# Performance work log

Measured on AMD Instinct MI355X. Metric: run time of the kernel, lower is better.

The kernel has to match this reference:

```python
import jax, jax.numpy as jnp
import numpy as np

B = 1024            # number of graphs
C = (64, 32, 16, 1) # args.channels
K = 25              # args.kernel_size
CUTOFF = 0.5        # args.cutoff
EPS = 1e-15


def gmm_conv(x, pos, n, g, mu, sigma, root, bias, out_ch):
    """GMMConv over a dynamically-built radius graph (dist<CUTOFF, no self loops),
    with mean aggregation, expressed densely per-graph (n in {5,25,75}).
    Equivalent to getA()+PyG GMMConv(aggr='mean') scatter/gather."""
    nb = pos.shape[0] // n
    posb = pos.reshape(nb, n, 2)
    # diff[b, s, t] = pos_t - pos_s  (edge (row=s, col=t): message flows s -> t)
    diff = posb[:, None, :, :] - posb[:, :, None, :]
    dist = jnp.linalg.norm(diff + 1e-12, axis=-1)            # [B,n,n]
    mask = (dist < CUTOFF) & (~jnp.eye(n, dtype=bool))       # [B,n,n]
    pseudo = diff / CUTOFF + 0.5                             # [B,n,n,2] edge_attr
    # Gaussian kernel weights: exp(-0.5 * sum_d (u_d - mu_kd)^2 / sigma_kd^2)
    gauss = jnp.exp(-0.5 * jnp.sum((pseudo[..., None, :] - mu) ** 2
                                   / (sigma ** 2 + EPS), axis=-1))  # [B,n,n,K]
    w = gauss * mask[..., None]
    xm = (x @ g).reshape(nb, n, K, out_ch)                   # source-transformed feats
    agg = jnp.einsum('bstk,bsko->bto', w, xm)                # scatter-sum into targets
    deg = jnp.maximum(jnp.sum(mask, axis=1), 1)              # in-degree per target [B,n]
    out = agg / deg[..., None].astype(x.dtype)               # mean aggregation
    return out.reshape(-1, out_ch) + x @ root + bias


def setup_inputs() -> dict:
    key = jax.random.key(0)
    ks = jax.random.split(key, 40)
    inp = {}
    inp['x'] = jax.random.normal(ks[0], (B * 5, C[0]), jnp.float32)
    inp['pos'] = jax.random.uniform(ks[1], (B * 5, 2), jnp.float32)

    def conv_params(k, fin, fout):
        k1, k2, k3, k4, k5 = jax.random.split(k, 5)
        g = jax.random.normal(k1, (fin, K * fout), jnp.float32) / np.sqrt(fin)
        mu = jax.random.normal(k2, (K, 2), jnp.float32)
        sigma = jax.random.uniform(k3, (K, 2), jnp.float32, minval=0.5, maxval=1.5)
        root = jax.random.normal(k4, (fin, fout), jnp.float32) / np.sqrt(fin)
        bias = jax.random.normal(k5, (fout,), jnp.float32) * 0.01
        return g, mu, sigma, root, bias

    for i, (fin, fout) in enumerate([(C[0], 5 * C[1]), (C[1], 3 * C[2]), (C[2], C[3])], 1):
        g, mu, sigma, root, bias = conv_params(ks[1 + i], fin, fout)
        inp[f'g{i}'], inp[f'mu{i}'], inp[f'sig{i}'] = g, mu, sigma
        inp[f'root{i}'], inp[f'cb{i}'] = root, bias

    def lin(k, fin, fout):
        kw, kb = jax.random.split(k)
        return (jax.random.normal(kw, (fin, fout), jnp.float32) / np.sqrt(fin),
                jax.random.normal(kb, (fout,), jnp.float32) * 0.01)

    for j, (pre, dims) in enumerate([('p1', (2 + C[1], 128, 64, 2)),
                                     ('p2', (2 + C[2], 128, 64, 2))]):
        for li in range(3):
            w, b_ = lin(ks[10 + 3 * j + li], dims[li], dims[li + 1])
            inp[f'{pre}w{li+1}'], inp[f'{pre}b{li+1}'] = w, b_
    return inp


def reference(x, pos, g1, mu1, sig1, root1, cb1, g2, mu2, sig2, root2, cb2,
              g3, mu3, sig3, root3, cb3,
              p1w1, p1b1, p1w2, p1b2, p1w3, p1b3,
              p2w1, p2b1, p2w2, p2b2, p2w3, p2b3):
    elu = jax.nn.elu
    # stage 1: 5 nodes/graph, conv expands node count x5
    x = elu(gmm_conv(x, pos, 5, g1, mu1, sig1, root1, cb1, 5 * C[1])).reshape(-1, C[1])
    p = jnp.concatenate([jnp.repeat(pos, 5, axis=0), x], axis=1)
    p = elu(p @ p1w1 + p1b1)
    p = elu(p @ p1w2 + p1b2)
    pos = elu(p @ p1w3 + p1b3)
    # stage 2: 25 nodes/graph, conv expands node count x3
    x = elu(gmm_conv(x, pos, 25, g2, mu2, sig2, root2, cb2, 3 * C[2])).reshape(-1, C[2])
    p = jnp.concatenate([jnp.repeat(pos, 3, axis=0), x], axis=1)
    p = elu(p @ p2w1 + p2b1)
    p = elu(p @ p2w2 + p2b2)
    pos = elu(p @ p2w3 + p2b3)
    # stage 3: 75 nodes/graph
    x = jnp.tanh(gmm_conv(x, pos, 75, g3, mu3, sig3, root3, cb3, C[3])).reshape(-1, C[3])
    return x, pos
```

## Files before the change

### kernel.cpp

```cpp
#include <hip/hip_runtime.h>
#include <math.h>


__device__ __forceinline__ float eluf(float v) { return v > 0.f ? v : __expf(v) - 1.f; }

#define NLOG2E_HALF (-0.72134752f)

__global__ __launch_bounds__(512) void conv1_kernel(
    const float* __restrict__ x, const float* __restrict__ pos,
    const float* __restrict__ g, const float* __restrict__ mu, const float* __restrict__ sig,
    const float* __restrict__ root, const float* __restrict__ bias,
    float* __restrict__ xout)
{
  const int b = blockIdx.x, tid = threadIdx.x;
  __shared__ __align__(16) float s_xT[64 * 12];
  __shared__ __align__(16) float s_xm[10 * 832];
  __shared__ __align__(16) float s_w[2 * 5 * 5 * 28];
  __shared__ __align__(16) float s_red[2 * 2 * 5 * 160];
  __shared__ float s_pos[20];
  __shared__ float s_msc[25][4];
  __shared__ float s_ideg[10];

  if (tid < 20) s_pos[tid] = pos[b * 20 + tid];
  if (tid < 25) {
    float m0 = mu[2 * tid], m1 = mu[2 * tid + 1];
    float s0 = sig[2 * tid], s1 = sig[2 * tid + 1];
    s_msc[tid][0] = 0.5f - m0;
    s_msc[tid][1] = 0.5f - m1;
    s_msc[tid][2] = NLOG2E_HALF / (s0 * s0 + 1e-15f);
    s_msc[tid][3] = NLOG2E_HALF / (s1 * s1 + 1e-15f);
  }
  for (int e = tid; e < 640; e += 512) { int nd = e >> 6, i = e & 63; s_xT[i * 12 + nd] = x[b * 640 + nd * 64 + i]; }
  for (int e = tid; e < 320; e += 512) { int r = e / 32, c = e % 32; s_xm[r * 832 + 800 + c] = 0.f; }
  __syncthreads();

  if (tid < 10) {
    int gg = tid / 5, t = tid % 5, c = 0;
    for (int s = 0; s < 5; ++s) {
      if (s == t) continue;
      float d0 = s_pos[(gg * 5 + t) * 2]     - s_pos[(gg * 5 + s) * 2]     + 1e-12f;
      float d1 = s_pos[(gg * 5 + t) * 2 + 1] - s_pos[(gg * 5 + s) * 2 + 1] + 1e-12f;
      c += (d0 * d0 + d1 * d1 < 0.25f) ? 1 : 0;
    }
    s_ideg[tid] = 1.f / (float)(c < 1 ? 1 : c);
  }
  for (int e = tid; e < 1400; e += 512) {
    int gg = e / 700, r2 = e % 700, t = r2 / 140, c = r2 % 140;
    int ch = c / 28, skl = c % 28;
    float wv = 0.f;
    if (skl < 25) {
      int kk = skl / 5, s = skl % 5, k = ch * 5 + kk;
      float d0 = s_pos[(gg * 5 + t) * 2]     - s_pos[(gg * 5 + s) * 2];
      float d1 = s_pos[(gg * 5 + t) * 2 + 1] - s_pos[(gg * 5 + s) * 2 + 1];
      float e0 = d0 + 1e-12f, e1 = d1 + 1e-12f;
      bool m = (e0 * e0 + e1 * e1 < 0.25f) && (s != t);
      float q0 = fmaf(2.f, d0, s_msc[k][0]);
      float q1 = fmaf(2.f, d1, s_msc[k][1]);
      float a = q0 * q0 * s_msc[k][2];
      a = fmaf(q1 * q1, s_msc[k][3], a);
// ... 39 lines not shown
    }
    __syncthreads();
    if (tid < 320) {
#define C1_STEP(SK0) { \
      float2 m0 = *(const float2*)&s_xm[(sg * 5 + ((SK0) % 5)) * 832 + ((SK0) / 5) * 160 + so0]; \
      float2 m1 = *(const float2*)&s_xm[(sg * 5 + (((SK0) + 1) % 5)) * 832 + (((SK0) + 1) / 5) * 160 + so0]; \
      float2 m2 = *(const float2*)&s_xm[(sg * 5 + (((SK0) + 2) % 5)) * 832 + (((SK0) + 2) / 5) * 160 + so0]; \
      float2 m3 = *(const float2*)&s_xm[(sg * 5 + (((SK0) + 3) % 5)) * 832 + (((SK0) + 3) / 5) * 160 + so0]; \
      _Pragma("unroll") \
      for (int t = 0; t < 5; ++t) { \
        const float4 wv = *(const float4*)&s_w[((sg * 5 + t) * 5 + ch) * 28 + (SK0)]; \
        sacc[t][0] = fmaf(wv.x, m0.x, sacc[t][0]); sacc[t][1] = fmaf(wv.x, m0.y, sacc[t][1]); \
        sacc[t][0] = fmaf(wv.y, m1.x, sacc[t][0]); sacc[t][1] = fmaf(wv.y, m1.y, sacc[t][1]); \
        sacc[t][0] = fmaf(wv.z, m2.x, sacc[t][0]); sacc[t][1] = fmaf(wv.z, m2.y, sacc[t][1]); \
        sacc[t][0] = fmaf(wv.w, m3.x, sacc[t][0]); sacc[t][1] = fmaf(wv.w, m3.y, sacc[t][1]); \
      } }
      if (sks == 0) { C1_STEP(0) C1_STEP(4) C1_STEP(8) C1_STEP(12) }
      else          { C1_STEP(16) C1_STEP(20) C1_STEP(24) }
#undef C1_STEP
    }
    __syncthreads();
  }

  if (tid < 400) {
    const int rb = tid / 80, cb = tid % 80;
    const int r0 = rb * 2, c0 = cb * 2;
    float a00 = 0.f, a01 = 0.f, a10 = 0.f, a11 = 0.f;
    #pragma unroll 4
    for (int i = 0; i < 64; ++i) {
      float2 rv = *(const float2*)(root + i * 160 + c0);
      float2 xv = *(const float2*)&s_xT[i * 12 + r0];
      a00 = fmaf(xv.x, rv.x, a00); a01 = fmaf(xv.x, rv.y, a01);
      a10 = fmaf(xv.y, rv.x, a10); a11 = fmaf(xv.y, rv.y, a11);
    }
    *(float2*)&s_xm[r0 * 832 + c0]       = make_float2(a00, a01);
    *(float2*)&s_xm[(r0 + 1) * 832 + c0] = make_float2(a10, a11);
  }
  if (tid < 320) {
    #pragma unroll
    for (int t = 0; t < 5; ++t) {
      s_red[((sks * 2 + sg) * 5 + t) * 160 + so0]     = sacc[t][0];
      s_red[((sks * 2 + sg) * 5 + t) * 160 + so0 + 1] = sacc[t][1];
    }
  }
  __syncthreads();
  for (int e = tid; e < 1600; e += 512) {
    int gg = e / 800, r2 = e % 800, t = r2 / 160, o = r2 % 160;
    float v = s_red[(gg * 5 + t) * 160 + o] + s_red[((2 + gg) * 5 + t) * 160 + o];
    v = v * s_ideg[gg * 5 + t] + s_xm[(gg * 5 + t) * 832 + o] + bias[o];
    xout[b * 1600 + e] = eluf(v);
  }
}

__global__ __launch_bounds__(320) void conv2_kernel(
    const float* __restrict__ x, const float* __restrict__ pos,
    const float* __restrict__ g, const float* __restrict__ mu, const float* __restrict__ sig,
    const float* __restrict__ root, const float* __restrict__ bias,
    float* __restrict__ xout)
{
  const int b = blockIdx.x, tid = threadIdx.x;
  __shared__ __align__(16) float s_xT[32 * 28];
  __shared__ __align__(16) float s_xm[125 * 52];
  __shared__ __align__(16) float s_w[25 * 132];
  __shared__ __align__(8)  float2 s_u[25 * 26];
  __shared__ float s_ek[25 * 5];
  __shared__ float s_pos[50];
  __shared__ float s_ideg[25];

  if (tid < 50) s_pos[tid] = pos[b * 50 + tid];
  if (tid < 25) {
    float m0 = mu[2 * tid], m1 = mu[2 * tid + 1];
    float sg0 = sig[2 * tid], sg1 = sig[2 * tid + 1];
    float n0 = NLOG2E_HALF / (sg0 * sg0 + 1e-15f);
    float n1 = NLOG2E_HALF / (sg1 * sg1 + 1e-15f);
    float c0 = 0.5f - m0, c1 = 0.5f - m1;
    s_ek[tid * 5 + 0] = n0;
    s_ek[tid * 5 + 1] = n1;
    s_ek[tid * 5 + 2] = 2.f * n0 * c0;
    s_ek[tid * 5 + 3] = 2.f * n1 * c1;
    s_ek[tid * 5 + 4] = fmaf(n0, c0 * c0, n1 * c1 * c1);
  }
  for (int e = tid; e < 800; e += 320) { int r = e / 32, i = e % 32; s_xT[i * 28 + r] = x[b * 800 + e]; }
  __syncthreads();

  for (int e = tid; e < 625; e += 320) {
    int t = e / 25, s = e % 25;
    float d0 = s_pos[t * 2]     - s_pos[s * 2];
    float d1 = s_pos[t * 2 + 1] - s_pos[s * 2 + 1];
    float e0 = d0 + 1e-12f, e1 = d1 + 1e-12f;
    bool m = (e0 * e0 + e1 * e1 < 0.25f) && (s != t);
    s_u[t * 26 + s] = m ? make_float2(2.f * d0, 2.f * d1) : make_float2(1e18f, 0.f);
  }
  if (tid < 25) {
    int t = tid, c = 0;
    for (int s = 0; s < 25; ++s) {
      if (s == t) continue;
      float d0 = s_pos[t * 2]     - s_pos[s * 2]     + 1e-12f;
      float d1 = s_pos[t * 2 + 1] - s_pos[s * 2 + 1] + 1e-12f;
      c += (d0 * d0 + d1 * d1 < 0.25f) ? 1 : 0;
    }
    s_ideg[t] = 1.f / (float)(c < 1 ? 1 : c);
  }
  __syncthreads();

  const bool act = tid < 300;
  const int grp = tid / 60, rr = tid % 60, tg = rr / 12, og = rr % 12;
  const int o0 = og * 4;
  const int t0 = tg * 5, sk0 = grp * 25, s0 = tg * 5;

  float acc2[5][4];
  #pragma unroll
  for (int tt = 0; tt < 5; ++tt) { acc2[tt][0] = acc2[tt][1] = acc2[tt][2] = acc2[tt][3] = 0.f; }

  for (int ch = 0; ch < 5; ++ch) {
    const int k0 = ch * 5;
    for (int e = tid; e < 3125; e += 320) {
      int t = e / 125, c = e % 125;
      int kk = c / 25, s = c % 25, k = k0 + kk;
      float2 uv = s_u[t * 26 + s];
      const float* ekp = &s_ek[k * 5];
      float ar = fmaf(uv.x * uv.x, ekp[0],
                 fmaf(uv.y * uv.y, ekp[1],
                 fmaf(uv.x, ekp[2],
                 fmaf(uv.y, ekp[3], ekp[4]))));
      s_w[t * 132 + c] = exp2f(ar);
    }
    if (act) {
      const float* gp = g + (k0 + grp) * 48 + o0;
      float a[5][4];
      #pragma unroll
      for (int r = 0; r < 5; ++r) { a[r][0] = a[r][1] = a[r][2] = a[r][3] = 0.f; }
      #pragma unroll 4
      for (int i = 0; i < 32; ++i) {
        float4 gv = *(const float4*)(gp + i * 1200);
        float x0 = s_xT[i * 28 + s0];
        float x1 = s_xT[i * 28 + s0 + 1];
        float x2 = s_xT[i * 28 + s0 + 2];
        float x3 = s_xT[i * 28 + s0 + 3];
        float x4 = s_xT[i * 28 + s0 + 4];
        a[0][0] = fmaf(x0, gv.x, a[0][0]); a[0][1] = fmaf(x0, gv.y, a[0][1]);
        a[0][2] = fmaf(x0, gv.z, a[0][2]); a[0][3] = fmaf(x0, gv.w, a[0][3]);
        a[1][0] = fmaf(x1, gv.x, a[1][0]); a[1][1] = fmaf(x1, gv.y, a[1][1]);
        a[1][2] = fmaf(x1, gv.z, a[1][2]); a[1][3] = fmaf(x1, gv.w, a[1][3]);
        a[2][0] = fmaf(x2, gv.x, a[2][0]); a[2][1] = fmaf(x2, gv.y, a[2][1]);
        a[2][2] = fmaf(x2, gv.z, a[2][2]); a[2][3] = fmaf(x2, gv.w, a[2][3]);
        a[3][0] = fmaf(x3, gv.x, a[3][0]); a[3][1] = fmaf(x3, gv.y, a[3][1]);
        a[3][2] = fmaf(x3, gv.z, a[3][2]); a[3][3] = fmaf(x3, gv.w, a[3][3]);
        a[4][0] = fmaf(x4, gv.x, a[4][0]); a[4][1] = fmaf(x4, gv.y, a[4][1]);
        a[4][2] = fmaf(x4, gv.z, a[4][2]); a[4][3] = fmaf(x4, gv.w, a[4][3]);
      }
      #pragma unroll
      for (int j = 0; j < 5; ++j)
        *(float4*)&s_xm[(grp * 25 + s0 + j) * 52 + o0] = make_float4(a[j][0], a[j][1], a[j][2], a[j][3]);
    }
    __syncthreads();
    if (act) {
      #pragma unroll 5
      for (int q = 0; q < 25; ++q) {
        const int sk = sk0 + q;
        float4 mv = *(const float4*)&s_xm[sk * 52 + o0];
        float w0 = s_w[(t0 + 0) * 132 + sk];
        float w1 = s_w[(t0 + 1) * 132 + sk];
        float w2 = s_w[(t0 + 2) * 132 + sk];
        float w3 = s_w[(t0 + 3) * 132 + sk];
        float w4 = s_w[(t0 + 4) * 132 + sk];
        acc2[0][0] = fmaf(w0, mv.x, acc2[0][0]); acc2[0][1] = fmaf(w0, mv.y, acc2[0][1]);
        acc2[0][2] = fmaf(w0, mv.z, acc2[0][2]); acc2[0][3] = fmaf(w0, mv.w, acc2[0][3]);
        acc2[1][0] = fmaf(w1, mv.x, acc2[1][0]); acc2[1][1] = fmaf(w1, mv.y, acc2[1][1]);
        acc2[1][2] = fmaf(w1, mv.z, acc2[1][2]); acc2[1][3] = fmaf(w1, mv.w, acc2[1][3]);
        acc2[2][0] = fmaf(w2, mv.x, acc2[2][0]); acc2[2][1] = fmaf(w2, mv.y, acc2[2][1]);
        acc2[2][2] = fmaf(w2, mv.z, acc2[2][2]); acc2[2][3] = fmaf(w2, mv.w, acc2[2][3]);
        acc2[3][0] = fmaf(w3, mv.x, acc2[3][0]); acc2[3][1] = fmaf(w3, mv.y, acc2[3][1]);
        acc2[3][2] = fmaf(w3, mv.z, acc2[3][2]); acc2[3][3] = fmaf(w3, mv.w, acc2[3][3]);
        acc2[4][0] = fmaf(w4, mv.x, acc2[4][0]); acc2[4][1] = fmaf(w4, mv.y, acc2[4][1]);
        acc2[4][2] = fmaf(w4, mv.z, acc2[4][2]); acc2[4][3] = fmaf(w4, mv.w, acc2[4][3]);
      }
    }
    __syncthreads();
  }

  if (act) {
    #pragma unroll
    for (int tt = 0; tt < 5; ++tt)
      *(float4*)&s_xm[grp * 1200 + (t0 + tt) * 48 + o0] =
          make_float4(acc2[tt][0], acc2[tt][1], acc2[tt][2], acc2[tt][3]);
  }
  __syncthreads();
  for (int e = tid; e < 1200; e += 320) {
    int t = e / 48, o = e % 48;
    float v = s_xm[e] + s_xm[1200 + e] + s_xm[2400 + e] + s_xm[3600 + e] + s_xm[4800 + e];
    v *= s_ideg[t];
    #pragma unroll 8
    for (int i = 0; i < 32; ++i) v = fmaf(s_xT[i * 28 + t], root[i * 48 + o], v);
    xout[b * 1200 + e] = eluf(v + bias[o]);
  }
}

__global__ __launch_bounds__(384) void conv3_kernel(
    const float* __restrict__ x, const float* __restrict__ pos,
    const float* __restrict__ g, const float* __restrict__ mu, const float* __restrict__ sig,
    const float* __restrict__ root, const float* __restrict__ bias,
    float* __restrict__ xout)
{
  const int b = blockIdx.x, tid = threadIdx.x;
  __shared__ __align__(8) float2 s_u[75 * 75];
  __shared__ float s_xm[75 * 28];
  __shared__ float s_x[75 * 16];
  __shared__ float s_g3[400];
  __shared__ float s_pos[150];
  __shared__ float s_ek[25 * 5];
  __shared__ float s_ideg[75];
  __shared__ float s_out[75];
  __shared__ float s_r3[16];

  if (tid < 150) s_pos[tid] = pos[b * 150 + tid];
  for (int e = tid; e < 1200; e += 384) s_x[e] = x[b * 1200 + e];
  for (int e = tid; e < 400; e += 384) s_g3[e] = g[e];
  if (tid < 25) {
    float m0 = mu[2 * tid], m1 = mu[2 * tid + 1];
    float sg0 = sig[2 * tid], sg1 = sig[2 * tid + 1];
    float n0 = NLOG2E_HALF / (sg0 * sg0 + 1e-15f);
    float n1 = NLOG2E_HALF / (sg1 * sg1 + 1e-15f);
    float c0 = 0.5f - m0, c1 = 0.5f - m1;
    s_ek[tid * 5 + 0] = n0;
    s_ek[tid * 5 + 1] = n1;
    s_ek[tid * 5 + 2] = 2.f * n0 * c0;
    s_ek[tid * 5 + 3] = 2.f * n1 * c1;
    s_ek[tid * 5 + 4] = n0 * c0 * c0 + n1 * c1 * c1;
  }
  if (tid < 16) s_r3[tid] = root[tid];
  if (tid < 75) s_out[tid] = 0.f;
  __syncthreads();

  for (int e = tid; e < 1875; e += 384) {
    int s = e / 25, k = e % 25;
    float a = 0.f;
    #pragma unroll
    for (int i = 0; i < 16; ++i) a = fmaf(s_x[s * 16 + i], s_g3[i * 25 + k], a);
    s_xm[s * 28 + k] = a;
  }
  for (int e = tid; e < 5625; e += 384) {
    int t = e / 75, s = e % 75;
    float d0 = s_pos[t * 2]     - s_pos[s * 2];
    float d1 = s_pos[t * 2 + 1] - s_pos[s * 2 + 1];
    float e0 = d0 + 1e-12f, e1 = d1 + 1e-12f;
    bool m = (e0 * e0 + e1 * e1 < 0.25f) && (s != t);
    s_u[e] = m ? make_float2(2.f * d0, 2.f * d1) : make_float2(1e18f, 0.f);
  }
  if (tid < 75) {
    int t = tid, c = 0;
    for (int s = 0; s < 75; ++s) {
      if (s == t) continue;
      float d0 = s_pos[t * 2]     - s_pos[s * 2]     + 1e-12f;
      float d1 = s_pos[t * 2 + 1] - s_pos[s * 2 + 1] + 1e-12f;
      c += (d0 * d0 + d1 * d1 < 0.25f) ? 1 : 0;
    }
    s_ideg[t] = 1.f / (float)(c < 1 ? 1 : c);
  }
  __syncthreads();

  if (tid < 375) {
    const int t = tid / 5, kg = tid % 5;
    float n0[5], n1[5], e0[5], e1[5], f[5];
    #pragma unroll
    for (int j = 0; j < 5; ++j) {
      int k = kg * 5 + j;
      n0[j] = s_ek[k * 5 + 0]; n1[j] = s_ek[k * 5 + 1];
      e0[j] = s_ek[k * 5 + 2]; e1[j] = s_ek[k * 5 + 3];
      f[j]  = s_ek[k * 5 + 4];
    }
    float acc[5] = {0.f, 0.f, 0.f, 0.f, 0.f};
    for (int s = 0; s < 75; ++s) {
      float2 uv = s_u[t * 75 + s];
      float u00 = uv.x * uv.x, u11 = uv.y * uv.y;
      #pragma unroll
      for (int j = 0; j < 5; ++j) {
        float ar = fmaf(u00, n0[j], fmaf(u11, n1[j], fmaf(uv.x, e0[j], fmaf(uv.y, e1[j], f[j]))));
        acc[j] = fmaf(exp2f(ar), s_xm[s * 28 + kg * 5 + j], acc[j]);
      }
    }
    float sum = acc[0] + acc[1] + acc[2] + acc[3] + acc[4];
    atomicAdd(&s_out[t], sum);
  }
  __syncthreads();

  if (tid < 75) {
    int t = tid;
    float r = 0.f;
    #pragma unroll
    for (int i = 0; i < 16; ++i) r = fmaf(s_x[t * 16 + i], s_r3[i], r);
    xout[b * 75 + t] = tanhf(s_out[t] * s_ideg[t] + r + bias[0]);
  }
}

__global__ __launch_bounds__(256) void mlp_kernel(
    const float* __restrict__ pos_src, const float* __restrict__ feat,
    const float* __restrict__ w1, const float* __restrict__ b1,
    const float* __restrict__ w2, const float* __restrict__ b2,
    const float* __restrict__ w3, const float* __restrict__ b3,
    float* __restrict__ out, int fdim, int rep)
{
  const int tid = threadIdx.x;
  const int row0 = blockIdx.x * 64;
  const int din = fdim + 2;
  __shared__ __align__(16) float s_inT[34][68];
  __shared__ __align__(16) float s_h1T[128][68];
  __shared__ __align__(16) float s_h2T[64][68];

  if (tid < 128) {
    int r = tid >> 1, d = tid & 1;
    s_inT[d][r] = pos_src[((row0 + r) / rep) * 2 + d];
  }
  for (int e = tid; e < 64 * fdim; e += 256) {
    int r = e / fdim, c = e % fdim;
    s_inT[2 + c][r] = feat[(row0 + r) * fdim + c];
  }
  __syncthreads();

  {
    const int rb = tid >> 4, jb = tid & 15;
    const int r0 = rb << 2, j0 = jb << 3;
    float acc[4][8];
    #pragma unroll
    for (int jj = 0; jj < 8; ++jj) {
      float bv = b1[j0 + jj];
      acc[0][jj] = bv; acc[1][jj] = bv; acc[2][jj] = bv; acc[3][jj] = bv;
    }
    for (int i = 0; i < din; ++i) {
      float4 xa = *(const float4*)&s_inT[i][r0];
      float4 wa = *(const float4*)(w1 + i * 128 + j0);
      float4 wb = *(const float4*)(w1 + i * 128 + j0 + 4);
      float wv[8] = {wa.x, wa.y, wa.z, wa.w, wb.x, wb.y, wb.z, wb.w};
      #pragma unroll
      for (int jj = 0; jj < 8; ++jj) {
        acc[0][jj] = fmaf(xa.x, wv[jj], acc[0][jj]);
        acc[1][jj] = fmaf(xa.y, wv[jj], acc[1][jj]);
        acc[2][jj] = fmaf(xa.z, wv[jj], acc[2][jj]);
        acc[3][jj] = fmaf(xa.w, wv[jj], acc[3][jj]);
      }
    }
    #pragma unroll
    for (int jj = 0; jj < 8; ++jj)
      *(float4*)&s_h1T[j0 + jj][r0] =
        make_float4(eluf(acc[0][jj]), eluf(acc[1][jj]), eluf(acc[2][jj]), eluf(acc[3][jj]));
  }
  __syncthreads();

  {
    const int rb = tid >> 4, jb = tid & 15;
    const int r0 = rb << 2, j0 = jb << 2;
    float acc[4][4];
    #pragma unroll
    for (int jj = 0; jj < 4; ++jj) {
      float bv = b2[j0 + jj];
      acc[0][jj] = bv; acc[1][jj] = bv; acc[2][jj] = bv; acc[3][jj] = bv;
    }
    #pragma unroll 4
    for (int i = 0; i < 128; ++i) {
      float4 ha = *(const float4*)&s_h1T[i][r0];
      float4 wa = *(const float4*)(w2 + i * 64 + j0);
      float wv[4] = {wa.x, wa.y, wa.z, wa.w};
      #pragma unroll
      for (int jj = 0; jj < 4; ++jj) {
        acc[0][jj] = fmaf(ha.x, wv[jj], acc[0][jj]);
        acc[1][jj] = fmaf(ha.y, wv[jj], acc[1][jj]);
        acc[2][jj] = fmaf(ha.z, wv[jj], acc[2][jj]);
        acc[3][jj] = fmaf(ha.w, wv[jj], acc[3][jj]);
      }
    }
    #pragma unroll
    for (int jj = 0; jj < 4; ++jj)
      *(float4*)&s_h2T[j0 + jj][r0] =
        make_float4(eluf(acc[0][jj]), eluf(acc[1][jj]), eluf(acc[2][jj]), eluf(acc[3][jj]));
  }
  __syncthreads();

  if (tid < 128) {
    int r = tid >> 1, c = tid & 1;
    float a = b3[c];
    #pragma unroll 8
    for (int j = 0; j < 64; ++j)
      a = fmaf(s_h2T[j][r], w3[j * 2 + c], a);
    out[(row0 + r) * 2 + c] = eluf(a);
  }
}

extern "C" void kernel_launch(void* const* d_in, const int* in_sizes, int n_in,
                              void* d_out, int out_size, void* d_ws, size_t ws_size,
                              hipStream_t stream)
{
  const float* x     = (const float*)d_in[0];
  const float* pos   = (const float*)d_in[1];
  const float* g1    = (const float*)d_in[2];
  const float* mu1   = (const float*)d_in[3];
  const float* sig1  = (const float*)d_in[4];
  const float* root1 = (const float*)d_in[5];
  const float* cb1   = (const float*)d_in[6];
  const float* g2    = (const float*)d_in[7];
  const float* mu2   = (const float*)d_in[8];
  const float* sig2  = (const float*)d_in[9];
  const float* root2 = (const float*)d_in[10];
  const float* cb2   = (const float*)d_in[11];
  const float* g3    = (const float*)d_in[12];
  const float* mu3   = (const float*)d_in[13];
  const float* sig3  = (const float*)d_in[14];
  const float* root3 = (const float*)d_in[15];
  const float* cb3   = (const float*)d_in[16];
  const float* p1w1  = (const float*)d_in[17];
  const float* p1b1  = (const float*)d_in[18];
  const float* p1w2  = (const float*)d_in[19];
  const float* p1b2  = (const float*)d_in[20];
  const float* p1w3  = (const float*)d_in[21];
  const float* p1b3  = (const float*)d_in[22];
  const float* p2w1  = (const float*)d_in[23];
  const float* p2b1  = (const float*)d_in[24];
  const float* p2w2  = (const float*)d_in[25];
  const float* p2b2  = (const float*)d_in[26];
  const float* p2w3  = (const float*)d_in[27];
  const float* p2b3  = (const float*)d_in[28];

  float* out  = (float*)d_out;
  float* ws   = (float*)d_ws;
  float* x1   = ws;
  float* pos1 = ws + 819200;
  float* x2   = ws + 870400;
  float* x3   = out;
  float* pos2 = out + 76800;

  conv1_kernel<<<dim3(512), dim3(512), 0, stream>>>(x, pos, g1, mu1, sig1, root1, cb1, x1);
  mlp_kernel<<<dim3(400), dim3(256), 0, stream>>>(pos, x1, p1w1, p1b1, p1w2, p1b2, p1w3, p1b3,
                                                  pos1, 32, 5);
  conv2_kernel<<<dim3(1024), dim3(320), 0, stream>>>(x1, pos1, g2, mu2, sig2, root2, cb2, x2);
  mlp_kernel<<<dim3(1200), dim3(256), 0, stream>>>(pos1, x2, p2w1, p2b1, p2w2, p2b2, p2w3, p2b3,
                                                  pos2, 16, 3);
  conv3_kernel<<<dim3(1024), dim3(384), 0, stream>>>(x2, pos2, g3, mu3, sig3, root3, cb3, x3);
}
```

Before: 336.6 us.

## Warp-specialize conv2 with double-buffered per-kernel build, shrink MLP tiles, recompute conv3 edges

Conv2 now splits its threads into roles. Threads 128 and up build the Gaussian weights and the transformed features for the next kernel component into a second buffer, while the first 128 threads accumulate the current component. This replaces the old five-chunk loop that carried two barriers per chunk, and it cuts shared memory use. The MLP kernel moves to 32-row tiles so it launches twice as many blocks with a smaller shared footprint. Conv3 drops its precomputed 75x75 edge array and recomputes the pairwise offsets inline to save shared memory. The trade-off is 25 barrier-separated iterations, with only 120 of 256 threads doing the accumulation.

```diff
diff --git a/kernel.cpp b/kernel.cpp
--- a/kernel.cpp
+++ b/kernel.cpp
@@ -5,6 +5,10 @@
 __device__ __forceinline__ float eluf(float v) { return v > 0.f ? v : __expf(v) - 1.f; }
 
 #define NLOG2E_HALF (-0.72134752f)
+
+#define FMA4(A, S, V) \
+  A.x = fmaf(S, V.x, A.x); A.y = fmaf(S, V.y, A.y); \
+  A.z = fmaf(S, V.z, A.z); A.w = fmaf(S, V.w, A.w);
 
 __global__ __launch_bounds__(512) void conv1_kernel(
     const float* __restrict__ x, const float* __restrict__ pos,
@@ -150,22 +154,26 @@
   }
 }
 
-__global__ __launch_bounds__(320) void conv2_kernel(
+__global__ __launch_bounds__(256) void conv2_kernel(
     const float* __restrict__ x, const float* __restrict__ pos,
     const float* __restrict__ g, const float* __restrict__ mu, const float* __restrict__ sig,
     const float* __restrict__ root, const float* __restrict__ bias,
     float* __restrict__ xout)
 {
   const int b = blockIdx.x, tid = threadIdx.x;
-  __shared__ __align__(16) float s_xT[32 * 28];
-  __shared__ __align__(16) float s_xm[125 * 52];
-  __shared__ __align__(16) float s_w[25 * 132];
+  __shared__ __align__(16) float s_x[25 * 36];
+  __shared__ __align__(16) float s_xm[2 * 28 * 52];
+  __shared__ __align__(16) float s_w[2 * 25 * 28];
   __shared__ __align__(8)  float2 s_u[25 * 26];
-  __shared__ float s_ek[25 * 5];
-  __shared__ float s_pos[50];
+  __shared__ float s_ek[125];
   __shared__ float s_ideg[25];
 
-  if (tid < 50) s_pos[tid] = pos[b * 50 + tid];
+  const float* posb = pos + b * 50;
+  for (int e = tid; e < 800; e += 256) s_x[(e >> 5) * 36 + (e & 31)] = x[b * 800 + e];
+  for (int e = tid; e < 312; e += 256) {
+    int q = e / 52, cc = e % 52;
+    s_xm[(q / 3) * 1456 + (25 + q % 3) * 52 + cc] = 0.f;
+  }
   if (tid < 25) {
     float m0 = mu[2 * tid], m1 = mu[2 * tid + 1];
     float sg0 = sig[2 * tid], sg1 = sig[2 * tid + 1];
@@ -178,13 +186,10 @@
     s_ek[tid * 5 + 3] = 2.f * n1 * c1;
     s_ek[tid * 5 + 4] = fmaf(n0, c0 * c0, n1 * c1 * c1);
   }
-  for (int e = tid; e < 800; e += 320) { int r = e / 32, i = e % 32; s_xT[i * 28 + r] = x[b * 800 + e]; }
-  __syncthreads();
-
-  for (int e = tid; e < 625; e += 320) {
+  for (int e = tid; e < 625; e += 256) {
     int t = e / 25, s = e % 25;
-    float d0 = s_pos[t * 2]     - s_pos[s * 2];
-    float d1 = s_pos[t * 2 + 1] - s_pos[s * 2 + 1];
+    float d0 = posb[t * 2]     - posb[s * 2];
+    float d1 = posb[t * 2 + 1] - posb[s * 2 + 1];
     float e0 = d0 + 1e-12f, e1 = d1 + 1e-12f;
     bool m = (e0 * e0 + e1 * e1 < 0.25f) && (s != t);
     s_u[t * 26 + s] = m ? make_float2(2.f * d0, 2.f * d1) : make_float2(1e18f, 0.f);
@@ -193,104 +198,102 @@
     int t = tid, c = 0;
     for (int s = 0; s < 25; ++s) {
       if (s == t) continue;
-      float d0 = s_pos[t * 2]     - s_pos[s * 2]     + 1e-12f;
-      float d1 = s_pos[t * 2 + 1] - s_pos[s * 2 + 1] + 1e-12f;
+      float d0 = posb[t * 2]     - posb[s * 2]     + 1e-12f;
+      float d1 = posb[t * 2 + 1] - posb[s * 2 + 1] + 1e-12f;
       c += (d0 * d0 + d1 * d1 < 0.25f) ? 1 : 0;
     }
     s_ideg[t] = 1.f / (float)(c < 1 ? 1 : c);
   }
   __syncthreads();
 
-  const bool act = tid < 300;
-  const int grp = tid / 60, rr = tid % 60, tg = rr / 12, og = rr % 12;
-  const int o0 = og * 4;
-  const int t0 = tg * 5, sk0 = grp * 25, s0 = tg * 5;
-
-  float acc2[5][4];
+  const bool scatA = tid < 60;
+  const bool scatB = (tid >= 64 && tid < 124);
+  const int srole = scatA ? tid : (scatB ? tid - 64 : 0);
+  const int st0 = (srole / 12) * 5, so0 = (srole % 12) * 4;
+  const int bt = tid - 128;
+
+#define C2_BUILD(C_, BUF_) { \
+  const int wOffB = (BUF_) * 700, xmOffB = (BUF_) * 1456; \
+  const float n0 = s_ek[(C_) * 5 + 0], n1 = s_ek[(C_) * 5 + 1]; \
+  const float ce0 = s_ek[(C_) * 5 + 2], ce1 = s_ek[(C_) * 5 + 3], cf = s_ek[(C_) * 5 + 4]; \
+  for (int e = bt; e < 700; e += 128) { \
+    int t = e / 28, s = e - t * 28; \
+    float wv = 0.f; \
+    if (s < 25) { \
+      float2 uv = s_u[t * 26 + s]; \
+      wv = exp2f(fmaf(uv.x * uv.x, n0, fmaf(uv.y * uv.y, n1, \
+                 fmaf(uv.x, ce0, fmaf(uv.y, ce1, cf))))); \
+    } \
+    s_w[wOffB + e] = wv; \
+  } \
+  const float* gc = g + (C_) * 48; \
+  for (int task = bt; task < 300; task += 128) { \
+    int s = task / 12, o0 = (task - s * 12) * 4; \
+    const float* gp = gc + o0; \
+    const float* xr = &s_x[s * 36]; \
+    float4 a = make_float4(0.f, 0.f, 0.f, 0.f); \
+    _Pragma("unroll") \
+    for (int i = 0; i < 32; i += 4) { \
+      float4 x4 = *(const float4*)(xr + i); \
+      float4 g0 = *(const float4*)(gp + (i + 0) * 1200); \
+      float4 g1 = *(const float4*)(gp + (i + 1) * 1200); \
+      float4 g2 = *(const float4*)(gp + (i + 2) * 1200); \
+      float4 g3 = *(const float4*)(gp + (i + 3) * 1200); \
+      FMA4(a, x4.x, g0) FMA4(a, x4.y, g1) FMA4(a, x4.z, g2) FMA4(a, x4.w, g3) \
+    } \
+    *(float4*)&s_xm[xmOffB + s * 52 + o0] = a; \
+  } }
+
+#define C2_STEP(SK0) { \
+  const float* mp = &s_xm[bufOff + (SK0) * 52 + so0]; \
+  float4 m0 = *(const float4*)(mp); \
+  float4 m1 = *(const float4*)(mp + 52); \
+  float4 m2 = *(const float4*)(mp + 104); \
+  float4 m3 = *(const float4*)(mp + 156); \
+  _Pragma("unroll") \
+  for (int tt = 0; tt < 5; ++tt) { \
+    float4 wv = *(const float4*)&s_w[wOff + (st0 + tt) * 28 + (SK0)]; \
+    FMA4(acc[tt], wv.x, m0) \
+    FMA4(acc[tt], wv.y, m1) \
+    FMA4(acc[tt], wv.z, m2) \
+    FMA4(acc[tt], wv.w, m3) \
+  } }
+
+  float4 acc[5];
   #pragma unroll
-  for (int tt = 0; tt < 5; ++tt) { acc2[tt][0] = acc2[tt][1] = acc2[tt][2] = acc2[tt][3] = 0.f; }
-
-  for (int ch = 0; ch < 5; ++ch) {
-    const int k0 = ch * 5;
-    for (int e = tid; e < 3125; e += 320) {
-      int t = e / 125, c = e % 125;
-      int kk = c / 25, s = c % 25, k = k0 + kk;
-      float2 uv = s_u[t * 26 + s];
-      const float* ekp = &s_ek[k * 5];
-      float ar = fmaf(uv.x * uv.x, ekp[0],
-                 fmaf(uv.y * uv.y, ekp[1],
-                 fmaf(uv.x, ekp[2],
-                 fmaf(uv.y, ekp[3], ekp[4]))));
-      s_w[t * 132 + c] = exp2f(ar);
-    }
-    if (act) {
-      const float* gp = g + (k0 + grp) * 48 + o0;
-      float a[5][4];
-      #pragma unroll
-      for (int r = 0; r < 5; ++r) { a[r][0] = a[r][1] = a[r][2] = a[r][3] = 0.f; }
-      #pragma unroll 4
-      for (int i = 0; i < 32; ++i) {
-        float4 gv = *(const float4*)(gp + i * 1200);
-        float x0 = s_xT[i * 28 + s0];
-        float x1 = s_xT[i * 28 + s0 + 1];
-        float x2 = s_xT[i * 28 + s0 + 2];
-        float x3 = s_xT[i * 28 + s0 + 3];
-        float x4 = s_xT[i * 28 + s0 + 4];
-        a[0][0] = fmaf(x0, gv.x, a[0][0]); a[0][1] = fmaf(x0, gv.y, a[0][1]);
-        a[0][2] = fmaf(x0, gv.z, a[0][2]); a[0][3] = fmaf(x0, gv.w, a[0][3]);
-        a[1][0] = fmaf(x1, gv.x, a[1][0]); a[1][1] = fmaf(x1, gv.y, a[1][1]);
-        a[1][2] = fmaf(x1, gv.z, a[1][2]); a[1][3] = fmaf(x1, gv.w, a[1][3]);
-        a[2][0] = fmaf(x2, gv.x, a[2][0]); a[2][1] = fmaf(x2, gv.y, a[2][1]);
-        a[2][2] = fmaf(x2, gv.z, a[2][2]); a[2][3] = fmaf(x2, gv.w, a[2][3]);
-        a[3][0] = fmaf(x3, gv.x, a[3][0]); a[3][1] = fmaf(x3, gv.y, a[3][1]);
-        a[3][2] = fmaf(x3, gv.z, a[3][2]); a[3][3] = fmaf(x3, gv.w, a[3][3]);
-        a[4][0] = fmaf(x4, gv.x, a[4][0]); a[4][1] = fmaf(x4, gv.y, a[4][1]);
-        a[4][2] = fmaf(x4, gv.z, a[4][2]); a[4][3] = fmaf(x4, gv.w, a[4][3]);
-      }
-      #pragma unroll
-      for (int j = 0; j < 5; ++j)
-        *(float4*)&s_xm[(grp * 25 + s0 + j) * 52 + o0] = make_float4(a[j][0], a[j][1], a[j][2], a[j][3]);
+  for (int tt = 0; tt < 5; ++tt) acc[tt] = make_float4(0.f, 0.f, 0.f, 0.f);
+
+  if (tid >= 128) { C2_BUILD(0, 0) }
+  __syncthreads();
+
+  for (int c = 0; c < 25; ++c) {
+    const int cur = c & 1;
+    if (tid < 128) {
+      const int bufOff = cur * 1456, wOff = cur * 700;
+      if (scatA)      { C2_STEP(0) C2_STEP(4) C2_STEP(8) C2_STEP(12) }
+      else if (scatB) { C2_STEP(16) C2_STEP(20) C2_STEP(24) }
+    } else if (c < 24) {
+      C2_BUILD(c + 1, cur ^ 1)
     }
     __syncthreads();
-    if (act) {
-      #pragma unroll 5
-      for (int q = 0; q < 25; ++q) {
-        const int sk = sk0 + q;
-        float4 mv = *(const float4*)&s_xm[sk * 52 + o0];
-        float w0 = s_w[(t0 + 0) * 132 + sk];
-        float w1 = s_w[(t0 + 1) * 132 + sk];
-        float w2 = s_w[(t0 + 2) * 132 + sk];
-        float w3 = s_w[(t0 + 3) * 132 + sk];
-        float w4 = s_w[(t0 + 4) * 132 + sk];
-        acc2[0][0] = fmaf(w0, mv.x, acc2[0][0]); acc2[0][1] = fmaf(w0, mv.y, acc2[0][1]);
-        acc2[0][2] = fmaf(w0, mv.z, acc2[0][2]); acc2[0][3] = fmaf(w0, mv.w, acc2[0][3]);
-        acc2[1][0] = fmaf(w1, mv.x, acc2[1][0]); acc2[1][1] = fmaf(w1, mv.y, acc2[1][1]);
-        acc2[1][2] = fmaf(w1, mv.z, acc2[1][2]); acc2[1][3] = fmaf(w1, mv.w, acc2[1][3]);
-        acc2[2][0] = fmaf(w2, mv.x, acc2[2][0]); acc2[2][1] = fmaf(w2, mv.y, acc2[2][1]);
-        acc2[2][2] = fmaf(w2, mv.z, acc2[2][2]); acc2[2][3] = fmaf(w2, mv.w, acc2[2][3]);
-        acc2[3][0] = fmaf(w3, mv.x, acc2[3][0]); acc2[3][1] = fmaf(w3, mv.y, acc2[3][1]);
-        acc2[3][2] = fmaf(w3, mv.z, acc2[3][2]); acc2[3][3] = fmaf(w3, mv.w, acc2[3][3]);
-        acc2[4][0] = fmaf(w4, mv.x, acc2[4][0]); acc2[4][1] = fmaf(w4, mv.y, acc2[4][1]);
-        acc2[4][2] = fmaf(w4, mv.z, acc2[4][2]); acc2[4][3] = fmaf(w4, mv.w, acc2[4][3]);
-      }
-    }
-    __syncthreads();
-  }
-
-  if (act) {
+  }
+#undef C2_STEP
+#undef C2_BUILD
+
+  if (scatA || scatB) {
+    const int h = scatA ? 0 : 1;
     #pragma unroll
     for (int tt = 0; tt < 5; ++tt)
-      *(float4*)&s_xm[grp * 1200 + (t0 + tt) * 48 + o0] =
-          make_float4(acc2[tt][0], acc2[tt][1], acc2[tt][2], acc2[tt][3]);
-  }
-  __syncthreads();
-  for (int e = tid; e < 1200; e += 320) {
-    int t = e / 48, o = e % 48;
-    float v = s_xm[e] + s_xm[1200 + e] + s_xm[2400 + e] + s_xm[3600 + e] + s_xm[4800 + e];
-    v *= s_ideg[t];
+      *(float4*)&s_xm[h * 1200 + (st0 + tt) * 48 + so0] = acc[tt];
+  }
+  __syncthreads();
+  for (int e = tid; e < 1200; e += 256) {
+    int t = e / 48, o = e - t * 48;
+    float v = fmaf(s_xm[e] + s_xm[1200 + e], s_ideg[t], bias[o]);
+    const float* xr = &s_x[t * 36];
     #pragma unroll 8
-    for (int i = 0; i < 32; ++i) v = fmaf(s_xT[i * 28 + t], root[i * 48 + o], v);
-    xout[b * 1200 + e] = eluf(v + bias[o]);
+    for (int i = 0; i < 32; ++i) v = fmaf(xr[i], root[i * 48 + o], v);
+    xout[b * 1200 + e] = eluf(v);
   }
 }
 
@@ -301,12 +304,11 @@
     float* __restrict__ xout)
 {
   const int b = blockIdx.x, tid = threadIdx.x;
-  __shared__ __align__(8) float2 s_u[75 * 75];
   __shared__ float s_xm[75 * 28];
   __shared__ float s_x[75 * 16];
   __shared__ float s_g3[400];
-  __shared__ float s_pos[150];
-  __shared__ float s_ek[25 * 5];
+  __shared__ __align__(8) float s_pos[150];
+  __shared__ float s_ek[125];
   __shared__ float s_ideg[75];
   __shared__ float s_out[75];
   __shared__ float s_r3[16];
@@ -337,14 +339,6 @@
     for (int i = 0; i < 16; ++i) a = fmaf(s_x[s * 16 + i], s_g3[i * 25 + k], a);
     s_xm[s * 28 + k] = a;
   }
-  for (int e = tid; e < 5625; e += 384) {
-    int t = e / 75, s = e % 75;
-    float d0 = s_pos[t * 2]     - s_pos[s * 2];
-    float d1 = s_pos[t * 2 + 1] - s_pos[s * 2 + 1];
-    float e0 = d0 + 1e-12f, e1 = d1 + 1e-12f;
-    bool m = (e0 * e0 + e1 * e1 < 0.25f) && (s != t);
-    s_u[e] = m ? make_float2(2.f * d0, 2.f * d1) : make_float2(1e18f, 0.f);
-  }
   if (tid < 75) {
     int t = tid, c = 0;
     for (int s = 0; s < 75; ++s) {
@@ -367,18 +361,23 @@
       e0[j] = s_ek[k * 5 + 2]; e1[j] = s_ek[k * 5 + 3];
       f[j]  = s_ek[k * 5 + 4];
     }
-    float acc[5] = {0.f, 0.f, 0.f, 0.f, 0.f};
+    const float pt0 = s_pos[t * 2], pt1 = s_pos[t * 2 + 1];
+    float acc5[5] = {0.f, 0.f, 0.f, 0.f, 0.f};
     for (int s = 0; s < 75; ++s) {
-      float2 uv = s_u[t * 75 + s];
-      float u00 = uv.x * uv.x, u11 = uv.y * uv.y;
+      float2 pv = *(const float2*)&s_pos[s * 2];
+      float d0 = pt0 - pv.x, d1 = pt1 - pv.y;
+      float ea = d0 + 1e-12f, eb = d1 + 1e-12f;
+      bool m = (ea * ea + eb * eb < 0.25f) && (s != t);
+      float ux = m ? 2.f * d0 : 1e18f;
+      float uy = m ? 2.f * d1 : 0.f;
+      float u00 = ux * ux, u11 = uy * uy;
       #pragma unroll
       for (int j = 0; j < 5; ++j) {
-        float ar = fmaf(u00, n0[j], fmaf(u11, n1[j], fmaf(uv.x, e0[j], fmaf(uv.y, e1[j], f[j]))));
-        acc[j] = fmaf(exp2f(ar), s_xm[s * 28 + kg * 5 + j], acc[j]);
+        float ar = fmaf(u00, n0[j], fmaf(u11, n1[j], fmaf(ux, e0[j], fmaf(uy, e1[j], f[j]))));
+        acc5[j] = fmaf(exp2f(ar), s_xm[s * 28 + kg * 5 + j], acc5[j]);
       }
     }
-    float sum = acc[0] + acc[1] + acc[2] + acc[3] + acc[4];
-    atomicAdd(&s_out[t], sum);
+    atomicAdd(&s_out[t], acc5[0] + acc5[1] + acc5[2] + acc5[3] + acc5[4]);
   }
   __syncthreads();
 
@@ -399,67 +398,67 @@
     float* __restrict__ out, int fdim, int rep)
 {
   const int tid = threadIdx.x;
-  const int row0 = blockIdx.x * 64;
+  const int row0 = blockIdx.x * 32;
   const int din = fdim + 2;
-  __shared__ __align__(16) float s_inT[34][68];
-  __shared__ __align__(16) float s_h1T[128][68];
-  __shared__ __align__(16) float s_h2T[64][68];
-
-  if (tid < 128) {
+  __shared__ __align__(16) char smem[27648];
+  float* s_h1T = (float*)smem;
+  float* s_inT = (float*)(smem + 18432);
+  float* s_h2T = (float*)(smem + 18432);
+
+  if (tid < 64) {
     int r = tid >> 1, d = tid & 1;
-    s_inT[d][r] = pos_src[((row0 + r) / rep) * 2 + d];
-  }
-  for (int e = tid; e < 64 * fdim; e += 256) {
+    s_inT[d * 36 + r] = pos_src[((row0 + r) / rep) * 2 + d];
+  }
+  for (int e = tid; e < 32 * fdim; e += 256) {
     int r = e / fdim, c = e % fdim;
-    s_inT[2 + c][r] = feat[(row0 + r) * fdim + c];
-  }
-  __syncthreads();
-
+    s_inT[(2 + c) * 36 + r] = feat[(row0 + r) * fdim + c];
+  }
+  __syncthreads();
+
+  const int rb = tid / 32, jb = tid % 32;
   {
-    const int rb = tid >> 4, jb = tid & 15;
-    const int r0 = rb << 2, j0 = jb << 3;
-    float acc[4][8];
-    #pragma unroll
-    for (int jj = 0; jj < 8; ++jj) {
+    const int r0 = rb * 4, j0 = jb * 4;
+    float acc[4][4];
+    #pragma unroll
+    for (int jj = 0; jj < 4; ++jj) {
       float bv = b1[j0 + jj];
       acc[0][jj] = bv; acc[1][jj] = bv; acc[2][jj] = bv; acc[3][jj] = bv;
     }
     for (int i = 0; i < din; ++i) {
-      float4 xa = *(const float4*)&s_inT[i][r0];
-      float4 wa = *(const float4*)(w1 + i * 128 + j0);
-      float4 wb = *(const float4*)(w1 + i * 128 + j0 + 4);
-      float wv[8] = {wa.x, wa.y, wa.z, wa.w, wb.x, wb.y, wb.z, wb.w};
+      float4 xa = *(const float4*)&s_inT[i * 36 + r0];
+      float4 wa = *(const float4*)&w1[i * 128 + j0];
+      float wv[4] = {wa.x, wa.y, wa.z, wa.w};
       #pragma unroll
-      for (int jj = 0; jj < 8; ++jj) {
+      for (int jj = 0; jj < 4; ++jj) {
         acc[0][jj] = fmaf(xa.x, wv[jj], acc[0][jj]);
         acc[1][jj] = fmaf(xa.y, wv[jj], acc[1][jj]);
         acc[2][jj] = fmaf(xa.z, wv[jj], acc[2][jj]);
         acc[3][jj] = fmaf(xa.w, wv[jj], acc[3][jj]);
       }
     }
-    #pragma unroll
-    for (int jj = 0; jj < 8; ++jj)
-      *(float4*)&s_h1T[j0 + jj][r0] =
+    __syncthreads();
+    #pragma unroll
+    for (int jj = 0; jj < 4; ++jj)
+      *(float4*)&s_h1T[(j0 + jj) * 36 + r0] =
         make_float4(eluf(acc[0][jj]), eluf(acc[1][jj]), eluf(acc[2][jj]), eluf(acc[3][jj]));
   }
   __syncthreads();
 
   {
-    const int rb = tid >> 4, jb = tid & 15;
-    const int r0 = rb << 2, j0 = jb << 2;
-    float acc[4][4];
-    #pragma unroll
-    for (int jj = 0; jj < 4; ++jj) {
+    const int r0 = rb * 4, j0 = jb * 2;
+    float acc[4][2];
+    #pragma unroll
+    for (int jj = 0; jj < 2; ++jj) {
       float bv = b2[j0 + jj];
       acc[0][jj] = bv; acc[1][jj] = bv; acc[2][jj] = bv; acc[3][jj] = bv;
     }
     #pragma unroll 4
     for (int i = 0; i < 128; ++i) {
-      float4 ha = *(const float4*)&s_h1T[i][r0];
-      float4 wa = *(const float4*)(w2 + i * 64 + j0);
-      float wv[4] = {wa.x, wa.y, wa.z, wa.w};
+      float4 ha = *(const float4*)&s_h1T[i * 36 + r0];
+      float2 wa = *(const float2*)&w2[i * 64 + j0];
+      float wv[2] = {wa.x, wa.y};
       #pragma unroll
-      for (int jj = 0; jj < 4; ++jj) {
+      for (int jj = 0; jj < 2; ++jj) {
         acc[0][jj] = fmaf(ha.x, wv[jj], acc[0][jj]);
         acc[1][jj] = fmaf(ha.y, wv[jj], acc[1][jj]);
         acc[2][jj] = fmaf(ha.z, wv[jj], acc[2][jj]);
@@ -467,18 +466,18 @@
       }
     }
     #pragma unroll
-    for (int jj = 0; jj < 4; ++jj)
-      *(float4*)&s_h2T[j0 + jj][r0] =
+    for (int jj = 0; jj < 2; ++jj)
+      *(float4*)&s_h2T[(j0 + jj) * 36 + r0] =
         make_float4(eluf(acc[0][jj]), eluf(acc[1][jj]), eluf(acc[2][jj]), eluf(acc[3][jj]));
   }
   __syncthreads();
 
-  if (tid < 128) {
+  if (tid < 64) {
     int r = tid >> 1, c = tid & 1;
     float a = b3[c];
     #pragma unroll 8
     for (int j = 0; j < 64; ++j)
-      a = fmaf(s_h2T[j][r], w3[j * 2 + c], a);
+      a = fmaf(s_h2T[j * 36 + r], w3[j * 2 + c], a);
     out[(row0 + r) * 2 + c] = eluf(a);
   }
 }
@@ -526,10 +525,10 @@
   float* pos2 = out + 76800;
 
   conv1_kernel<<<dim3(512), dim3(512), 0, stream>>>(x, pos, g1, mu1, sig1, root1, cb1, x1);
-  mlp_kernel<<<dim3(400), dim3(256), 0, stream>>>(pos, x1, p1w1, p1b1, p1w2, p1b2, p1w3, p1b3,
+  mlp_kernel<<<dim3(800), dim3(256), 0, stream>>>(pos, x1, p1w1, p1b1, p1w2, p1b2, p1w3, p1b3,
                                                   pos1, 32, 5);
-  conv2_kernel<<<dim3(1024), dim3(320), 0, stream>>>(x1, pos1, g2, mu2, sig2, root2, cb2, x2);
-  mlp_kernel<<<dim3(1200), dim3(256), 0, stream>>>(pos1, x2, p2w1, p2b1, p2w2, p2b2, p2w3, p2b3,
+  conv2_kernel<<<dim3(1024), dim3(256), 0, stream>>>(x1, pos1, g2, mu2, sig2, root2, cb2, x2);
+  mlp_kernel<<<dim3(2400), dim3(256), 0, stream>>>(pos1, x2, p2w1, p2b1, p2w2, p2b2, p2w3, p2b3,
                                                   pos2, 16, 3);
   conv3_kernel<<<dim3(1024), dim3(384), 0, stream>>>(x2, pos2, g3, mu3, sig3, root3, cb3, x3);
 }
```

Result: slower. 351.8 us (+4.5%).

## Use neighbor lists in conv3, retile MLP to 32 rows, drop conv2 pos smem

Applied to the files above, without the earlier changes.

In conv3, each target now builds a compacted byte list of in-radius neighbours and loops only over those, recomputing the pseudo-coordinates from positions. This replaces the dense 75x75 float2 edge buffer and skips the Gaussian evaluation for masked pairs, reducing exp work and shared memory. The MLP kernel is retiled to 32 rows per block with aliased shared buffers, doubling the grid and raising occupancy. conv2 reads positions directly from global memory instead of staging them in shared memory. The neighbour-list loop has a per-target trip count, which adds divergence across lanes, and the MLP tiling adds an extra barrier.

```diff
diff --git a/kernel.cpp b/kernel.cpp
--- a/kernel.cpp
+++ b/kernel.cpp
@@ -5,6 +5,10 @@
 __device__ __forceinline__ float eluf(float v) { return v > 0.f ? v : __expf(v) - 1.f; }
 
 #define NLOG2E_HALF (-0.72134752f)
+
+#define FMA4(A, S, V) \
+  A.x = fmaf(S, V.x, A.x); A.y = fmaf(S, V.y, A.y); \
+  A.z = fmaf(S, V.z, A.z); A.w = fmaf(S, V.w, A.w);
 
 __global__ __launch_bounds__(512) void conv1_kernel(
     const float* __restrict__ x, const float* __restrict__ pos,
@@ -162,10 +166,9 @@
   __shared__ __align__(16) float s_w[25 * 132];
   __shared__ __align__(8)  float2 s_u[25 * 26];
   __shared__ float s_ek[25 * 5];
-  __shared__ float s_pos[50];
   __shared__ float s_ideg[25];
 
-  if (tid < 50) s_pos[tid] = pos[b * 50 + tid];
+  const float* posb = pos + b * 50;
   if (tid < 25) {
     float m0 = mu[2 * tid], m1 = mu[2 * tid + 1];
     float sg0 = sig[2 * tid], sg1 = sig[2 * tid + 1];
@@ -183,8 +186,8 @@
 
   for (int e = tid; e < 625; e += 320) {
     int t = e / 25, s = e % 25;
-    float d0 = s_pos[t * 2]     - s_pos[s * 2];
-    float d1 = s_pos[t * 2 + 1] - s_pos[s * 2 + 1];
+    float d0 = posb[t * 2]     - posb[s * 2];
+    float d1 = posb[t * 2 + 1] - posb[s * 2 + 1];
     float e0 = d0 + 1e-12f, e1 = d1 + 1e-12f;
     bool m = (e0 * e0 + e1 * e1 < 0.25f) && (s != t);
     s_u[t * 26 + s] = m ? make_float2(2.f * d0, 2.f * d1) : make_float2(1e18f, 0.f);
@@ -193,8 +196,8 @@
     int t = tid, c = 0;
     for (int s = 0; s < 25; ++s) {
       if (s == t) continue;
-      float d0 = s_pos[t * 2]     - s_pos[s * 2]     + 1e-12f;
-      float d1 = s_pos[t * 2 + 1] - s_pos[s * 2 + 1] + 1e-12f;
+      float d0 = posb[t * 2]     - posb[s * 2]     + 1e-12f;
+      float d1 = posb[t * 2 + 1] - posb[s * 2 + 1] + 1e-12f;
       c += (d0 * d0 + d1 * d1 < 0.25f) ? 1 : 0;
     }
     s_ideg[t] = 1.f / (float)(c < 1 ? 1 : c);
@@ -301,15 +304,16 @@
     float* __restrict__ xout)
 {
   const int b = blockIdx.x, tid = threadIdx.x;
-  __shared__ __align__(8) float2 s_u[75 * 75];
   __shared__ float s_xm[75 * 28];
   __shared__ float s_x[75 * 16];
   __shared__ float s_g3[400];
-  __shared__ float s_pos[150];
-  __shared__ float s_ek[25 * 5];
+  __shared__ __align__(8) float s_pos[150];
+  __shared__ float s_ek[125];
   __shared__ float s_ideg[75];
   __shared__ float s_out[75];
   __shared__ float s_r3[16];
+  __shared__ unsigned char s_adj[75 * 76];
+  __shared__ int s_cnt[75];
 
   if (tid < 150) s_pos[tid] = pos[b * 150 + tid];
   for (int e = tid; e < 1200; e += 384) s_x[e] = x[b * 1200 + e];
@@ -337,22 +341,16 @@
     for (int i = 0; i < 16; ++i) a = fmaf(s_x[s * 16 + i], s_g3[i * 25 + k], a);
     s_xm[s * 28 + k] = a;
   }
-  for (int e = tid; e < 5625; e += 384) {
-    int t = e / 75, s = e % 75;
-    float d0 = s_pos[t * 2]     - s_pos[s * 2];
-    float d1 = s_pos[t * 2 + 1] - s_pos[s * 2 + 1];
-    float e0 = d0 + 1e-12f, e1 = d1 + 1e-12f;
-    bool m = (e0 * e0 + e1 * e1 < 0.25f) && (s != t);
-    s_u[e] = m ? make_float2(2.f * d0, 2.f * d1) : make_float2(1e18f, 0.f);
-  }
   if (tid < 75) {
     int t = tid, c = 0;
+    float pt0 = s_pos[t * 2], pt1 = s_pos[t * 2 + 1];
     for (int s = 0; s < 75; ++s) {
       if (s == t) continue;
-      float d0 = s_pos[t * 2]     - s_pos[s * 2]     + 1e-12f;
-      float d1 = s_pos[t * 2 + 1] - s_pos[s * 2 + 1] + 1e-12f;
-      c += (d0 * d0 + d1 * d1 < 0.25f) ? 1 : 0;
-    }
+      float d0 = pt0 - s_pos[s * 2]     + 1e-12f;
+      float d1 = pt1 - s_pos[s * 2 + 1] + 1e-12f;
+      if (d0 * d0 + d1 * d1 < 0.25f) s_adj[t * 76 + (c++)] = (unsigned char)s;
+    }
+    s_cnt[t] = c;
     s_ideg[t] = 1.f / (float)(c < 1 ? 1 : c);
   }
   __syncthreads();
@@ -367,18 +365,24 @@
       e0[j] = s_ek[k * 5 + 2]; e1[j] = s_ek[k * 5 + 3];
       f[j]  = s_ek[k * 5 + 4];
     }
-    float acc[5] = {0.f, 0.f, 0.f, 0.f, 0.f};
-    for (int s = 0; s < 75; ++s) {
-      float2 uv = s_u[t * 75 + s];
-      float u00 = uv.x * uv.x, u11 = uv.y * uv.y;
+    const float pt0 = s_pos[t * 2], pt1 = s_pos[t * 2 + 1];
+    const int cnt = s_cnt[t];
+    const unsigned char* adj = &s_adj[t * 76];
+    float acc5[5] = {0.f, 0.f, 0.f, 0.f, 0.f};
+    for (int ii = 0; ii < cnt; ++ii) {
+      int s = adj[ii];
+      float2 pv = *(const float2*)&s_pos[s * 2];
+      float ux = 2.f * (pt0 - pv.x);
+      float uy = 2.f * (pt1 - pv.y);
+      float u00 = ux * ux, u11 = uy * uy;
+      const float* xmp = &s_xm[s * 28 + kg * 5];
       #pragma unroll
       for (int j = 0; j < 5; ++j) {
-        float ar = fmaf(u00, n0[j], fmaf(u11, n1[j], fmaf(uv.x, e0[j], fmaf(uv.y, e1[j], f[j]))));
-        acc[j] = fmaf(exp2f(ar), s_xm[s * 28 + kg * 5 + j], acc[j]);
+        float ar = fmaf(u00, n0[j], fmaf(u11, n1[j], fmaf(ux, e0[j], fmaf(uy, e1[j], f[j]))));
+        acc5[j] = fmaf(exp2f(ar), xmp[j], acc5[j]);
       }
     }
-    float sum = acc[0] + acc[1] + acc[2] + acc[3] + acc[4];
-    atomicAdd(&s_out[t], sum);
+    atomicAdd(&s_out[t], acc5[0] + acc5[1] + acc5[2] + acc5[3] + acc5[4]);
   }
   __syncthreads();
 
@@ -399,67 +403,67 @@
     float* __restrict__ out, int fdim, int rep)
 {
   const int tid = threadIdx.x;
-  const int row0 = blockIdx.x * 64;
+  const int row0 = blockIdx.x * 32;
   const int din = fdim + 2;
-  __shared__ __align__(16) float s_inT[34][68];
-  __shared__ __align__(16) float s_h1T[128][68];
-  __shared__ __align__(16) float s_h2T[64][68];
-
-  if (tid < 128) {
+  __shared__ __align__(16) char smem[27648];
+  float* s_h1T = (float*)smem;
+  float* s_inT = (float*)(smem + 18432);
+  float* s_h2T = (float*)(smem + 18432);
+
+  if (tid < 64) {
     int r = tid >> 1, d = tid & 1;
-    s_inT[d][r] = pos_src[((row0 + r) / rep) * 2 + d];
-  }
-  for (int e = tid; e < 64 * fdim; e += 256) {
+    s_inT[d * 36 + r] = pos_src[((row0 + r) / rep) * 2 + d];
+  }
+  for (int e = tid; e < 32 * fdim; e += 256) {
     int r = e / fdim, c = e % fdim;
-    s_inT[2 + c][r] = feat[(row0 + r) * fdim + c];
-  }
-  __syncthreads();
-
+    s_inT[(2 + c) * 36 + r] = feat[(row0 + r) * fdim + c];
+  }
+  __syncthreads();
+
+  const int rb = tid / 32, jb = tid % 32;
   {
-    const int rb = tid >> 4, jb = tid & 15;
-    const int r0 = rb << 2, j0 = jb << 3;
-    float acc[4][8];
-    #pragma unroll
-    for (int jj = 0; jj < 8; ++jj) {
+    const int r0 = rb * 4, j0 = jb * 4;
+    float acc[4][4];
+    #pragma unroll
+    for (int jj = 0; jj < 4; ++jj) {
       float bv = b1[j0 + jj];
       acc[0][jj] = bv; acc[1][jj] = bv; acc[2][jj] = bv; acc[3][jj] = bv;
     }
     for (int i = 0; i < din; ++i) {
-      float4 xa = *(const float4*)&s_inT[i][r0];
-      float4 wa = *(const float4*)(w1 + i * 128 + j0);
-      float4 wb = *(const float4*)(w1 + i * 128 + j0 + 4);
-      float wv[8] = {wa.x, wa.y, wa.z, wa.w, wb.x, wb.y, wb.z, wb.w};
-      #pragma unroll
-      for (int jj = 0; jj < 8; ++jj) {
+      float4 xa = *(const float4*)&s_inT[i * 36 + r0];
+      float4 wa = *(const float4*)&w1[i * 128 + j0];
+      float wv[4] = {wa.x, wa.y, wa.z, wa.w};
+      #pragma unroll
+      for (int jj = 0; jj < 4; ++jj) {
         acc[0][jj] = fmaf(xa.x, wv[jj], acc[0][jj]);
         acc[1][jj] = fmaf(xa.y, wv[jj], acc[1][jj]);
         acc[2][jj] = fmaf(xa.z, wv[jj], acc[2][jj]);
         acc[3][jj] = fmaf(xa.w, wv[jj], acc[3][jj]);
       }
     }
-    #pragma unroll
-    for (int jj = 0; jj < 8; ++jj)
-      *(float4*)&s_h1T[j0 + jj][r0] =
+    __syncthreads();
+    #pragma unroll
+    for (int jj = 0; jj < 4; ++jj)
+      *(float4*)&s_h1T[(j0 + jj) * 36 + r0] =
         make_float4(eluf(acc[0][jj]), eluf(acc[1][jj]), eluf(acc[2][jj]), eluf(acc[3][jj]));
   }
   __syncthreads();
 
   {
-    const int rb = tid >> 4, jb = tid & 15;
-    const int r0 = rb << 2, j0 = jb << 2;
-    float acc[4][4];
-    #pragma unroll
-    for (int jj = 0; jj < 4; ++jj) {
+    const int r0 = rb * 4, j0 = jb * 2;
+    float acc[4][2];
+    #pragma unroll
+    for (int jj = 0; jj < 2; ++jj) {
       float bv = b2[j0 + jj];
       acc[0][jj] = bv; acc[1][jj] = bv; acc[2][jj] = bv; acc[3][jj] = bv;
     }
     #pragma unroll 4
     for (int i = 0; i < 128; ++i) {
-      float4 ha = *(const float4*)&s_h1T[i][r0];
-      float4 wa = *(const float4*)(w2 + i * 64 + j0);
-      float wv[4] = {wa.x, wa.y, wa.z, wa.w};
-      #pragma unroll
-      for (int jj = 0; jj < 4; ++jj) {
+      float4 ha = *(const float4*)&s_h1T[i * 36 + r0];
+      float2 wa = *(const float2*)&w2[i * 64 + j0];
+      float wv[2] = {wa.x, wa.y};
+      #pragma unroll
+      for (int jj = 0; jj < 2; ++jj) {
         acc[0][jj] = fmaf(ha.x, wv[jj], acc[0][jj]);
         acc[1][jj] = fmaf(ha.y, wv[jj], acc[1][jj]);
         acc[2][jj] = fmaf(ha.z, wv[jj], acc[2][jj]);
@@ -467,18 +471,18 @@
       }
     }
     #pragma unroll
-    for (int jj = 0; jj < 4; ++jj)
-      *(float4*)&s_h2T[j0 + jj][r0] =
+    for (int jj = 0; jj < 2; ++jj)
+      *(float4*)&s_h2T[(j0 + jj) * 36 + r0] =
         make_float4(eluf(acc[0][jj]), eluf(acc[1][jj]), eluf(acc[2][jj]), eluf(acc[3][jj]));
   }
   __syncthreads();
 
-  if (tid < 128) {
+  if (tid < 64) {
     int r = tid >> 1, c = tid & 1;
     float a = b3[c];
     #pragma unroll 8
     for (int j = 0; j < 64; ++j)
-      a = fmaf(s_h2T[j][r], w3[j * 2 + c], a);
+      a = fmaf(s_h2T[j * 36 + r], w3[j * 2 + c], a);
     out[(row0 + r) * 2 + c] = eluf(a);
   }
 }
@@ -526,10 +530,10 @@
   float* pos2 = out + 76800;
 
   conv1_kernel<<<dim3(512), dim3(512), 0, stream>>>(x, pos, g1, mu1, sig1, root1, cb1, x1);
-  mlp_kernel<<<dim3(400), dim3(256), 0, stream>>>(pos, x1, p1w1, p1b1, p1w2, p1b2, p1w3, p1b3,
+  mlp_kernel<<<dim3(800), dim3(256), 0, stream>>>(pos, x1, p1w1, p1b1, p1w2, p1b2, p1w3, p1b3,
                                                   pos1, 32, 5);
   conv2_kernel<<<dim3(1024), dim3(320), 0, stream>>>(x1, pos1, g2, mu2, sig2, root2, cb2, x2);
-  mlp_kernel<<<dim3(1200), dim3(256), 0, stream>>>(pos1, x2, p2w1, p2b1, p2w2, p2b2, p2w3, p2b3,
+  mlp_kernel<<<dim3(2400), dim3(256), 0, stream>>>(pos1, x2, p2w1, p2b1, p2w2, p2b2, p2w3, p2b3,
                                                   pos2, 16, 3);
   conv3_kernel<<<dim3(1024), dim3(384), 0, stream>>>(x2, pos2, g3, mu3, sig3, root3, cb3, x3);
 }
```

Result: faster. 287.5 us, median of 2 (-14.6%).
